# Kernel tuning notes

Measured on AMD Instinct MI355X. Metric: run time of the kernel, lower is better.

The kernel has to match this reference:

```python
import jax, jax.numpy as jnp
import numpy as np

N_HEADS = 16
BLOCK_SIZE = 256


def setup_inputs() -> dict:
    key = jax.random.key(0)
    ks = jax.random.split(key, 5)
    B, T, C = 4, 4096, 1024
    scale = 0.02
    return {
        "x": jax.random.normal(ks[0], (B, T, C), dtype=jnp.float32),
        "Wqkv": jax.random.normal(ks[1], (C, 3 * C), dtype=jnp.float32) * scale,
        "bqkv": jnp.zeros((3 * C,), dtype=jnp.float32),
        "Wout": jax.random.normal(ks[2], (C, C), dtype=jnp.float32) * scale,
        "bout": jnp.zeros((C,), dtype=jnp.float32),
    }


def reference(x, Wqkv, bqkv, Wout, bout):
    B, T, C = x.shape
    H = N_HEADS
    hd = C // H
    bs = BLOCK_SIZE
    nb = T // bs

    qkv = x @ Wqkv + bqkv                     # [B,T,3C]
    qkv = qkv.reshape(B, T, H, 3 * hd).transpose(0, 2, 1, 3)  # [B,H,T,3hd]
    q, k, v = jnp.split(qkv, 3, axis=-1)      # each [B,H,T,hd]

    # block-diagonal local attention: reshape T -> (nb, bs)
    q = q.reshape(B, H, nb, bs, hd)
    k = k.reshape(B, H, nb, bs, hd)
    v = v.reshape(B, H, nb, bs, hd)

    scores = jnp.einsum("bhnqd,bhnkd->bhnqk", q, k) * (hd ** -0.5)
    attn = jax.nn.softmax(scores, axis=-1)
    o = jnp.einsum("bhnqk,bhnkd->bhnqd", attn, v)  # [B,H,nb,bs,hd]

    o = o.reshape(B, H, T, hd).transpose(0, 2, 1, 3).reshape(B, T, C)
    return o @ Wout + bout
```

## Files before the change

### kernel.cpp

```cpp
#include <hip/hip_runtime.h>

typedef unsigned int u32;
typedef unsigned long long u64;
typedef unsigned short u16;
typedef short bf16x8 __attribute__((ext_vector_type(8)));
typedef u16 u16x8 __attribute__((ext_vector_type(8)));
typedef float f32x4 __attribute__((ext_vector_type(4)));


__device__ __forceinline__ u16 f2bf(float f) {
  unsigned u = __float_as_uint(f);
  u += 0x7FFFu + ((u >> 16) & 1u);
  return (u16)(u >> 16);
}

typedef const void __attribute__((address_space(1)))* gas_p;
typedef void __attribute__((address_space(3)))* las_p;

__device__ __forceinline__ void async_ld16(const void* g, void* l) {
  __builtin_amdgcn_global_load_lds((gas_p)g, (las_p)l, 16, 0, 0);
}


__global__ __launch_bounds__(256) void k_prep(const float* __restrict__ x,
                                              u16* __restrict__ xb,
                                              const float* __restrict__ Wqkv,
                                              u16* __restrict__ wqkvT,
                                              const float* __restrict__ Wout,
                                              u16* __restrict__ woT) {
  __shared__ u16 tsh[32][33];
  int bid = blockIdx.x;
  int tid = threadIdx.x;

  if (bid < 8192) {
    int i = bid * 256 + tid;
    const float4* p = (const float4*)x + (size_t)i * 2;
    float4 a = p[0], b = p[1];
    u16x8 o;
    o[0] = f2bf(a.x); o[1] = f2bf(a.y); o[2] = f2bf(a.z); o[3] = f2bf(a.w);
    o[4] = f2bf(b.x); o[5] = f2bf(b.y); o[6] = f2bf(b.z); o[7] = f2bf(b.w);
    *((u16x8*)xb + i) = o;
    return;
  }

  const float* in;
  u16* out;
  int R, Ncols, bx, by;
  if (bid < 11264) {
    int t = bid - 8192;
    in = Wqkv; out = wqkvT; R = 1024; Ncols = 3072;
    bx = t % 96; by = t / 96;
  } else {
    int t = bid - 11264;
    in = Wout; out = woT; R = 1024; Ncols = 1024;
    bx = t & 31; by = t >> 5;
  }
  int tx = tid & 31, ty = tid >> 5;
  int c0 = bx * 32, r0 = by * 32;
#pragma unroll
  for (int j = 0; j < 32; j += 8)
    tsh[ty + j][tx] = f2bf(in[(size_t)(r0 + ty + j) * Ncols + c0 + tx]);
  __syncthreads();
#pragma unroll
  for (int j = 0; j < 32; j += 8)
    out[(size_t)(c0 + ty + j) * R + r0 + tx] = tsh[tx][ty + j];
}


#define STAGE_A2(h_, src_, dd_) do {                                       \
    const u16* g_ = (src_) + (size_t)(h_) * 128 * KK;                      \
    u16* s_ = lds + (dd_) * 16384 + (((h_) * 128 + w * 16) << 6);          \
    async_ld16(g_, s_);                                                    \
    async_ld16(g_ + 8 * (size_t)KK, s_ + 512);                             \
  } while (0)

#define STAGE_B2(h_, src_, dd_) do {                                       \
    const u16* g_ = (src_) + (size_t)(h_) * 128 * KK;                      \
    u16* s_ = lds + 32768 + (dd_) * 16384 + (((h_) * 128 + w * 16) << 6);  \
    async_ld16(g_, s_);                                                    \
    async_ld16(g_ + 8 * (size_t)KK, s_ + 512);                             \
  } while (0)

#define MQUAD(M0, N0)                                                      \
    _Pragma("unroll") for (int ks = 0; ks < 2; ++ks)                       \
    _Pragma("unroll") for (int mm = 0; mm < 4; ++mm)                       \
    _Pragma("unroll") for (int nn = 0; nn < 2; ++nn)                       \
      acc[(M0) + mm][(N0) + nn] = __builtin_amdgcn_mfma_f32_16x16x32_bf16( \
          a[(M0) + mm][ks], b[(N0) + nn][ks], acc[(M0) + mm][(N0) + nn], 0, 0, 0);

#define TBX(d_, bS_, aS_)                                                  \
  {                                                                        \
    const int doA = (d_) * 16384, doB = 32768 + (d_) * 16384;              \
      \
    _Pragma("unroll") for (int f = 0; f < 8; ++f) {                        \
      a[f][0] = *(const bf16x8*)(lds + doA + rAoff + f * 1024 + c0);       \
      a[f][1] = *(const bf16x8*)(lds + doA + rAoff + f * 1024 + c1);       \
    }                                                                      \
    _Pragma("unroll") for (int f = 0; f < 4; ++f) {                        \
      b[f][0] = *(const bf16x8*)(lds + doB + rBoff + f * 1024 + c0);       \
      b[f][1] = *(const bf16x8*)(lds + doB + rBoff + f * 1024 + c1);       \
    }                                                                      \
        \
    STAGE_B2(0, bS_, (d_) ^ 1);                                            \
    STAGE_B2(1, bS_, (d_) ^ 1);                                            \
                            \
    __builtin_amdgcn_s_setprio(1);                                         \
    MQUAD(0, 0)                                                            \
    MQUAD(4, 0)                                                            \
    __builtin_amdgcn_s_setprio(0);                                         \
        \
    __builtin_amdgcn_s_barrier();                                          \
    STAGE_A2(0, aS_, (d_));                                                \
    STAGE_A2(1, aS_, (d_));                                                \
    __builtin_amdgcn_s_setprio(1);                                         \
    MQUAD(0, 2)                                                            \
    MQUAD(4, 2)                                                            \
    __builtin_amdgcn_s_setprio(0);                                         \
    \
    asm volatile("s_waitcnt vmcnt(4)");                                    \
    __builtin_amdgcn_s_barrier();           \
  }

#define EPI(PM0, PN0) do {                                                      \
    int ccol0 = (PN0) + wn * 64 + (lane & 15);                                  \
    float bv0 = bias[ccol0], bv1 = bias[ccol0 + 16];                            \
    float bv2 = bias[ccol0 + 32], bv3 = bias[ccol0 + 48];                       \
    size_t crow0 = (size_t)((PM0) + wm * 128 + ((lane >> 4) << 2));             \
    _Pragma("unroll") for (int m = 0; m < 8; ++m)                               \
    _Pragma("unroll") for (int reg = 0; reg < 4; ++reg) {                       \
      size_t ro = (crow0 + m * 16 + reg) * (size_t)N + ccol0;                   \
      float v0 = acc[m][0][reg] + bv0, v1 = acc[m][1][reg] + bv1;               \
      float v2 = acc[m][2][reg] + bv2, v3 = acc[m][3][reg] + bv3;               \
      if (OUT_BF16) {                                                           \
        ((u16*)Cout)[ro] = f2bf(v0); ((u16*)Cout)[ro + 16] = f2bf(v1);          \
        ((u16*)Cout)[ro + 32] = f2bf(v2); ((u16*)Cout)[ro + 48] = f2bf(v3);     \
      } else {                                                                  \
        ((float*)Cout)[ro] = v0; ((float*)Cout)[ro + 16] = v1;                  \
        ((float*)Cout)[ro + 32] = v2; ((float*)Cout)[ro + 48] = v3;             \
      }                                                                         \
    }                                                                           \
  } while (0)

#define TILE_COORD(tt, mm0, nn0) do {                                           \
    int q_ = nwg >> 3, r_ = nwg & 7, x_ = (tt) & 7, loc_ = (tt) >> 3;           \
    int swz_ = (x_ < r_ ? x_ * (q_ + 1) : r_ * (q_ + 1) + (x_ - r_) * q_) + loc_;\
    mm0 = (swz_ / nbn) << 8; nn0 = (swz_ % nbn) << 8;                           \
  } while (0)

#define ZERO_ACC do {                                                           \
    _Pragma("unroll") for (int m = 0; m < 8; ++m)                               \
    _Pragma("unroll") for (int n = 0; n < 4; ++n)                               \
      acc[m][n] = (f32x4){0.f, 0.f, 0.f, 0.f};                                  \
  } while (0)

template <int OUT_BF16, int KK>
__global__ __launch_bounds__(512, 2) void k_gemm8(const u16* __restrict__ A,
                                                  const u16* __restrict__ Bt,
                                                  const float* __restrict__ bias,
                                                  void* __restrict__ Cout,
                                                  int M, int N) {
  extern __shared__ u16 lds[];
  const int NT = KK / 64;

  int nbn = N >> 8, nbm = M >> 8, nwg = nbm * nbn;
  int tid = threadIdx.x;
  int w = tid >> 6, lane = tid & 63;
  int wm = w >> 2, wn = w & 3;

  int rAoff = (wm * 128 + (lane & 15)) << 6;
  int rBoff = (wn * 64 + (lane & 15)) << 6;
  int hi8 = (lane >> 4) << 3, key8 = (lane & 7) << 3;
  int c0 = hi8 ^ key8;
  int c1 = (32 | hi8) ^ key8;
  int rowoff = w * 16 + (lane >> 3);
  int soff = ((lane & 7) ^ (lane >> 3)) << 3;

  bf16x8 a[8][2], b[4][2];
  f32x4 acc[8][4];

  int t = blockIdx.x;
  int m0, n0;
  TILE_COORD(t, m0, n0);
  const u16* pAg = A + (size_t)(m0 + rowoff) * KK + soff;
  const u16* pBg = Bt + (size_t)(n0 + rowoff) * KK + soff;

  STAGE_A2(0, pAg, 0); STAGE_A2(1, pAg, 0);
  STAGE_B2(0, pBg, 0); STAGE_B2(1, pBg, 0);
  STAGE_A2(0, pAg + 64, 1); STAGE_A2(1, pAg + 64, 1);
  asm volatile("s_waitcnt vmcnt(4)");
  __builtin_amdgcn_s_barrier();
  ZERO_ACC;

  for (;;) {
    int tn = t + gridDim.x;
    bool last = tn >= nwg;
    const u16 *pAgN, *pBgN;
    int m0N = m0, n0N = n0;
    if (last) {
      pAgN = pAg; pBgN = pBg;
    } else {
      TILE_COORD(tn, m0N, n0N);
      pAgN = A + (size_t)(m0N + rowoff) * KK + soff;
      pBgN = Bt + (size_t)(n0N + rowoff) * KK + soff;
    }

    for (int k = 0; k < NT; k += 2) {
      const u16* bS1 = pBg + (k + 1) * 64;
      const u16* aS2 = (k + 2 < NT) ? pAg + (k + 2) * 64 : pAgN + (k + 2 - NT) * 64;
      TBX(0, bS1, aS2)
      const u16* bS2 = (k + 2 < NT) ? pBg + (k + 2) * 64 : pBgN + (k + 2 - NT) * 64;
      const u16* aS3 = (k + 3 < NT) ? pAg + (k + 3) * 64 : pAgN + (k + 3 - NT) * 64;
      TBX(1, bS2, aS3)
    }

    EPI(m0, n0);
    if (last) break;
    t = tn; m0 = m0N; n0 = n0N; pAg = pAgN; pBg = pBgN;
    ZERO_ACC;
  }
  asm volatile("s_waitcnt vmcnt(0) lgkmcnt(0)");
}


__global__ __launch_bounds__(512, 4) void k_attn3(const u16* __restrict__ qkv,
                                                  u16* __restrict__ o) {
  __shared__ u16 ldsK[256 * 64];
  __shared__ u16 ldsV[64 * 256];

  int bid = blockIdx.x;
  int g = ((bid & 7) << 8) | (bid >> 3);
  int hq = g & 1, blk = (g >> 1) & 15, h = (g >> 5) & 15, b = g >> 9;

  int tid = threadIdx.x;
  int w = tid >> 6, lane = tid & 63;
  int hgrp = lane >> 4;
  size_t rowb = ((size_t)(b * 4096 + blk * 256)) * 3072 + (size_t)h * 192;

  int qrow = hq * 128 + w * 16 + (lane & 15);
  const u16* qp = qkv + rowb + (size_t)qrow * 3072 + hgrp * 8;
  bf16x8 qf0 = *(const bf16x8*)(qp);
  bf16x8 qf1 = *(const bf16x8*)(qp + 32);

#pragma unroll
  for (int it = 0; it < 4; ++it) {
    int trow = it * 64 + (tid >> 3);
    const u16* ksrc = qkv + rowb + (size_t)trow * 3072 + 64 +
                      (((lane & 7) ^ (lane >> 3)) << 3);
    async_ld16(ksrc, ldsK + (it * 64 + w * 8) * 64);
  }

  {
    int tg = tid >> 3, d0 = (tid & 7) << 3;
    const u16* vsrc = qkv + rowb + (size_t)(4 * tg) * 3072 + 128 + d0;
    union { uint4 v; u16 s[8]; } r0, r1, r2, r3;
    r0.v = *(const uint4*)(vsrc);
    r1.v = *(const uint4*)(vsrc + 3072);
    r2.v = *(const uint4*)(vsrc + 6144);
    r3.v = *(const uint4*)(vsrc + 9216);
    int gb = ((tg >> 1) << 4) + ((tg & 1) << 3);
#pragma unroll
    for (int c = 0; c < 8; ++c) {
      int d = d0 + c;
      int key = (((d & 7) ^ ((d >> 3) & 7)) & 7) << 4;
      u64 pack = (u64)r0.s[c] | ((u64)r1.s[c] << 16) |
                 ((u64)r2.s[c] << 32) | ((u64)r3.s[c] << 48);
      *(u64*)((char*)ldsV + d * 512 + ((gb & ~15) ^ key) + (gb & 8)) = pack;
    }
  }
  __syncthreads();

  f32x4 acc0[16] = {};
  int cb = hgrp << 4;
#pragma unroll
  for (int ct = 0; ct < 16; ++ct) {
    int krow = ct * 16 + (lane & 15);
    const char* kb = (const char*)ldsK + krow * 128;
    int key = (krow & 7) << 4;
    bf16x8 k0 = *(const bf16x8*)(kb + (cb ^ key));
    bf16x8 k1 = *(const bf16x8*)(kb + ((64 + cb) ^ key));
    acc0[ct] = __builtin_amdgcn_mfma_f32_16x16x32_bf16(k0, qf0, acc0[ct], 0, 0, 0);
    acc0[ct] = __builtin_amdgcn_mfma_f32_16x16x32_bf16(k1, qf1, acc0[ct], 0, 0, 0);
  }

  const float SC = 0.125f * 1.44269504f;
  float rden0;
  {
    float mx = -1e30f;
#pragma unroll
    for (int ct = 0; ct < 16; ++ct)
#pragma unroll
      for (int rg = 0; rg < 4; ++rg) mx = fmaxf(mx, acc0[ct][rg]);
    mx = fmaxf(mx, __shfl_xor(mx, 16));
    mx = fmaxf(mx, __shfl_xor(mx, 32));
    float s = 0.f;
#pragma unroll
    for (int ct = 0; ct < 16; ++ct)
#pragma unroll
      for (int rg = 0; rg < 4; ++rg) {
        float p = exp2f((acc0[ct][rg] - mx) * SC);
        acc0[ct][rg] = p;
        s += p;
      }
    s += __shfl_xor(s, 16);
    s += __shfl_xor(s, 32);
    rden0 = 1.f / s;
  }

  int s1 = (lane & 15) + ((lane >> 4) & 1) * 32;
  int s2 = s1 + 16;
  bool lo = (lane < 32);
  f32x4 oa[4] = {};
#pragma unroll
  for (int kt = 0; kt < 8; ++kt) {
    u32 wA0, wB0, wA1, wB1;
    asm("v_cvt_pk_bf16_f32 %0, %1, %2" : "=v"(wA0)
        : "v"(acc0[2 * kt][0]), "v"(acc0[2 * kt][1]));
    asm("v_cvt_pk_bf16_f32 %0, %1, %2" : "=v"(wB0)
        : "v"(acc0[2 * kt][2]), "v"(acc0[2 * kt][3]));
    asm("v_cvt_pk_bf16_f32 %0, %1, %2" : "=v"(wA1)
        : "v"(acc0[2 * kt + 1][0]), "v"(acc0[2 * kt + 1][1]));
    asm("v_cvt_pk_bf16_f32 %0, %1, %2" : "=v"(wB1)
        : "v"(acc0[2 * kt + 1][2]), "v"(acc0[2 * kt + 1][3]));
    u32 t0a = (u32)__shfl((int)wA0, s1), t0b = (u32)__shfl((int)wA1, s1);
    u32 t1a = (u32)__shfl((int)wB0, s1), t1b = (u32)__shfl((int)wB1, s1);
    u32 t2a = (u32)__shfl((int)wA0, s2), t2b = (u32)__shfl((int)wA1, s2);
    u32 t3a = (u32)__shfl((int)wB0, s2), t3b = (u32)__shfl((int)wB1, s2);
    union { u32 w[4]; bf16x8 v; } pu;
    pu.w[0] = lo ? t0a : t0b;
    pu.w[1] = lo ? t1a : t1b;
    pu.w[2] = lo ? t2a : t2b;
    pu.w[3] = lo ? t3a : t3b;
    bf16x8 pa = pu.v;
    int vkb = 2 * (kt * 32 + hgrp * 8);
#pragma unroll
    for (int nt = 0; nt < 4; ++nt) {
      int vd = nt * 16 + (lane & 15);
      int key = (((vd & 7) ^ ((vd >> 3) & 7)) & 7) << 4;
      bf16x8 vf = *(const bf16x8*)((char*)ldsV + vd * 512 + (vkb ^ key));
      oa[nt] = __builtin_amdgcn_mfma_f32_16x16x32_bf16(pa, vf, oa[nt], 0, 0, 0);
    }
  }

  float rd0[4];
#pragma unroll
  for (int rg = 0; rg < 4; ++rg) rd0[rg] = __shfl(rden0, 4 * hgrp + rg, 16);
  size_t ob = ((size_t)(b * 4096 + blk * 256 + hq * 128 + w * 16)) * 1024 +
              (size_t)h * 64;
#pragma unroll
  for (int nt = 0; nt < 4; ++nt)
#pragma unroll
    for (int rg = 0; rg < 4; ++rg) {
      int col = nt * 16 + (lane & 15);
      o[ob + (size_t)(4 * hgrp + rg) * 1024 + col] = f2bf(oa[nt][rg] * rd0[rg]);
    }
}


extern "C" void kernel_launch(void* const* d_in, const int* in_sizes, int n_in,
                              void* d_out, int out_size, void* d_ws, size_t ws_size,
                              hipStream_t stream) {
  (void)in_sizes; (void)n_in; (void)out_size; (void)ws_size;
  const float* x = (const float*)d_in[0];
  const float* Wqkv = (const float*)d_in[1];
  const float* bqkv = (const float*)d_in[2];
  const float* Wout = (const float*)d_in[3];
  const float* bout = (const float*)d_in[4];
  float* out = (float*)d_out;

  char* ws = (char*)d_ws;
  u16* xb    = (u16*)(ws + 0);
  u16* wqkvT = (u16*)(ws + 33554432);
  u16* woT   = (u16*)(ws + 39845888);
  u16* qkv   = (u16*)(ws + 41943040);
  u16* ob    = (u16*)(ws + 142606336);

  hipFuncSetAttribute(reinterpret_cast<const void*>(&k_gemm8<1, 1024>),
                      hipFuncAttributeMaxDynamicSharedMemorySize, 131072);
  hipFuncSetAttribute(reinterpret_cast<const void*>(&k_gemm8<0, 1024>),
                      hipFuncAttributeMaxDynamicSharedMemorySize, 131072);

  k_prep<<<12288, 256, 0, stream>>>(x, xb, Wqkv, wqkvT, Wout, woT);

  k_gemm8<1, 1024><<<256, 512, 131072, stream>>>(xb, wqkvT, bqkv, qkv, 16384, 3072);

  k_attn3<<<2048, 512, 0, stream>>>(qkv, ob);

  k_gemm8<0, 1024><<<256, 512, 131072, stream>>>(ob, woT, bout, out, 16384, 1024);
}
```

Measured before the change: 234.2 us.

## Rework GEMM to 4 waves with 128x128 per-wave tiles and staged LDS pipeline

Replaces the 8-wave 256x256 GEMM workgroup with a 4-wave version in which each wave computes a 128x128 output sub-tile (8x8 accumulator fragments). The K-step is split into four MFMA quadrants, with A/B fragment reloads and async global-to-LDS stages interleaved between barriers. The goal is more MFMA work per LDS fragment load and less per-wave overhead. The cost is a doubled accumulator register footprint with one workgroup per CU, which lowers occupancy and makes latency hiding depend on the hand-written interleaving.

```diff
diff --git a/kernel.cpp b/kernel.cpp
--- a/kernel.cpp
+++ b/kernel.cpp
@@ -67,76 +67,85 @@
 }
 
 
-#define STAGE_A2(h_, src_, dd_) do {                                       \
-    const u16* g_ = (src_) + (size_t)(h_) * 128 * KK;                      \
-    u16* s_ = lds + (dd_) * 16384 + (((h_) * 128 + w * 16) << 6);          \
-    async_ld16(g_, s_);                                                    \
-    async_ld16(g_ + 8 * (size_t)KK, s_ + 512);                             \
-  } while (0)
-
-#define STAGE_B2(h_, src_, dd_) do {                                       \
-    const u16* g_ = (src_) + (size_t)(h_) * 128 * KK;                      \
-    u16* s_ = lds + 32768 + (dd_) * 16384 + (((h_) * 128 + w * 16) << 6);  \
-    async_ld16(g_, s_);                                                    \
-    async_ld16(g_ + 8 * (size_t)KK, s_ + 512);                             \
-  } while (0)
-
-#define MQUAD(M0, N0)                                                      \
-    _Pragma("unroll") for (int ks = 0; ks < 2; ++ks)                       \
-    _Pragma("unroll") for (int mm = 0; mm < 4; ++mm)                       \
-    _Pragma("unroll") for (int nn = 0; nn < 2; ++nn)                       \
-      acc[(M0) + mm][(N0) + nn] = __builtin_amdgcn_mfma_f32_16x16x32_bf16( \
-          a[(M0) + mm][ks], b[(N0) + nn][ks], acc[(M0) + mm][(N0) + nn], 0, 0, 0);
-
-#define TBX(d_, bS_, aS_)                                                  \
-  {                                                                        \
-    const int doA = (d_) * 16384, doB = 32768 + (d_) * 16384;              \
-      \
-    _Pragma("unroll") for (int f = 0; f < 8; ++f) {                        \
-      a[f][0] = *(const bf16x8*)(lds + doA + rAoff + f * 1024 + c0);       \
-      a[f][1] = *(const bf16x8*)(lds + doA + rAoff + f * 1024 + c1);       \
-    }                                                                      \
-    _Pragma("unroll") for (int f = 0; f < 4; ++f) {                        \
-      b[f][0] = *(const bf16x8*)(lds + doB + rBoff + f * 1024 + c0);       \
-      b[f][1] = *(const bf16x8*)(lds + doB + rBoff + f * 1024 + c1);       \
-    }                                                                      \
+#define STAGE_A4(h_, src_, dd_) do {                                          \
+    _Pragma("unroll") for (int i_ = 0; i_ < 4; ++i_)                          \
+      async_ld16((src_) + (size_t)((h_) * 128 + i_ * 8) * KK,                 \
+                 lds + (dd_) * 16384 + (((h_) * 128 + w * 32 + i_ * 8) << 6));\
+  } while (0)
+
+#define STAGE_B4(h_, src_, dd_) do {                                          \
+    _Pragma("unroll") for (int i_ = 0; i_ < 4; ++i_)                          \
+      async_ld16((src_) + (size_t)((h_) * 128 + i_ * 8) * KK,                 \
+                 lds + 32768 + (dd_) * 16384 +                                \
+                     (((h_) * 128 + w * 32 + i_ * 8) << 6));                  \
+  } while (0)
+
+#define MQ(M0, N0)                                                            \
+    __builtin_amdgcn_s_setprio(1);                                            \
+    _Pragma("unroll") for (int ks = 0; ks < 2; ++ks)                          \
+    _Pragma("unroll") for (int mm = 0; mm < 4; ++mm)                          \
+    _Pragma("unroll") for (int nn = 0; nn < 4; ++nn)                          \
+      acc[(M0) + mm][(N0) + nn] = __builtin_amdgcn_mfma_f32_16x16x32_bf16(    \
+          a[(M0) + mm][ks], b[nn][ks], acc[(M0) + mm][(N0) + nn], 0, 0, 0);   \
+    __builtin_amdgcn_s_setprio(0);
+
+#define TBX(d_, bS_, aS_)                                                     \
+  {                                                                           \
+    const int doA = (d_) * 16384, doB = 32768 + (d_) * 16384;                 \
+                              \
+    _Pragma("unroll") for (int f = 0; f < 4; ++f) {                           \
+      a[f][0] = *(const bf16x8*)(lds + doA + rAoff + f * 1024 + c0);          \
+      a[f][1] = *(const bf16x8*)(lds + doA + rAoff + f * 1024 + c1);          \
+    }                                                                         \
+    _Pragma("unroll") for (int f = 0; f < 4; ++f) {                           \
+      b[f][0] = *(const bf16x8*)(lds + doB + rBoff + f * 1024 + c0);          \
+      b[f][1] = *(const bf16x8*)(lds + doB + rBoff + f * 1024 + c1);          \
+    }                                                                         \
+    STAGE_B4(0, bS_, (d_) ^ 1);                                               \
+    asm volatile("s_waitcnt lgkmcnt(8)");                                     \
+    __builtin_amdgcn_s_barrier();                                             \
+    asm volatile("s_waitcnt lgkmcnt(0)");                                     \
+    MQ(0, 0)                                                                  \
+    __builtin_amdgcn_s_barrier();                                             \
+                                          \
+    _Pragma("unroll") for (int f = 4; f < 8; ++f) {                           \
+      a[f][0] = *(const bf16x8*)(lds + doA + rAoff + f * 1024 + c0);          \
+      a[f][1] = *(const bf16x8*)(lds + doA + rAoff + f * 1024 + c1);          \
+    }                                                                         \
+    STAGE_B4(1, bS_, (d_) ^ 1);                                               \
+    __builtin_amdgcn_s_barrier();                                             \
+    asm volatile("s_waitcnt lgkmcnt(0)");                                     \
+    MQ(4, 0)                                                                  \
+    __builtin_amdgcn_s_barrier();                                             \
+                      \
+    _Pragma("unroll") for (int f = 0; f < 4; ++f) {                           \
+      b[f][0] = *(const bf16x8*)(lds + doB + rBoff + (f + 4) * 1024 + c0);    \
+      b[f][1] = *(const bf16x8*)(lds + doB + rBoff + (f + 4) * 1024 + c1);    \
+    }                                                                         \
+    STAGE_A4(0, aS_, (d_));                                                   \
+    __builtin_amdgcn_s_barrier();                                             \
+    asm volatile("s_waitcnt lgkmcnt(0)");                                     \
+    MQ(4, 4)                                                                  \
+    __builtin_amdgcn_s_barrier();                                             \
         \
-    STAGE_B2(0, bS_, (d_) ^ 1);                                            \
-    STAGE_B2(1, bS_, (d_) ^ 1);                                            \
-                            \
-    __builtin_amdgcn_s_setprio(1);                                         \
-    MQUAD(0, 0)                                                            \
-    MQUAD(4, 0)                                                            \
-    __builtin_amdgcn_s_setprio(0);                                         \
-        \
-    __builtin_amdgcn_s_barrier();                                          \
-    STAGE_A2(0, aS_, (d_));                                                \
-    STAGE_A2(1, aS_, (d_));                                                \
-    __builtin_amdgcn_s_setprio(1);                                         \
-    MQUAD(0, 2)                                                            \
-    MQUAD(4, 2)                                                            \
-    __builtin_amdgcn_s_setprio(0);                                         \
-    \
-    asm volatile("s_waitcnt vmcnt(4)");                                    \
-    __builtin_amdgcn_s_barrier();           \
+    STAGE_A4(1, aS_, (d_));                                                   \
+    MQ(0, 4)                                                                  \
+    asm volatile("s_waitcnt vmcnt(8)");                                       \
+    __builtin_amdgcn_s_barrier();                                             \
   }
 
 #define EPI(PM0, PN0) do {                                                      \
-    int ccol0 = (PN0) + wn * 64 + (lane & 15);                                  \
-    float bv0 = bias[ccol0], bv1 = bias[ccol0 + 16];                            \
-    float bv2 = bias[ccol0 + 32], bv3 = bias[ccol0 + 48];                       \
+    int ccol0 = (PN0) + wn * 128 + (lane & 15);                                 \
+    float bv[8];                                                                \
+    _Pragma("unroll") for (int n = 0; n < 8; ++n) bv[n] = bias[ccol0 + n * 16]; \
     size_t crow0 = (size_t)((PM0) + wm * 128 + ((lane >> 4) << 2));             \
     _Pragma("unroll") for (int m = 0; m < 8; ++m)                               \
     _Pragma("unroll") for (int reg = 0; reg < 4; ++reg) {                       \
       size_t ro = (crow0 + m * 16 + reg) * (size_t)N + ccol0;                   \
-      float v0 = acc[m][0][reg] + bv0, v1 = acc[m][1][reg] + bv1;               \
-      float v2 = acc[m][2][reg] + bv2, v3 = acc[m][3][reg] + bv3;               \
-      if (OUT_BF16) {                                                           \
-        ((u16*)Cout)[ro] = f2bf(v0); ((u16*)Cout)[ro + 16] = f2bf(v1);          \
-        ((u16*)Cout)[ro + 32] = f2bf(v2); ((u16*)Cout)[ro + 48] = f2bf(v3);     \
-      } else {                                                                  \
-        ((float*)Cout)[ro] = v0; ((float*)Cout)[ro + 16] = v1;                  \
-        ((float*)Cout)[ro + 32] = v2; ((float*)Cout)[ro + 48] = v3;             \
+      _Pragma("unroll") for (int n = 0; n < 8; ++n) {                           \
+        float v = acc[m][n][reg] + bv[n];                                       \
+        if (OUT_BF16) ((u16*)Cout)[ro + n * 16] = f2bf(v);                      \
+        else          ((float*)Cout)[ro + n * 16] = v;                          \
       }                                                                         \
     }                                                                           \
   } while (0)
@@ -149,34 +158,34 @@
 
 #define ZERO_ACC do {                                                           \
     _Pragma("unroll") for (int m = 0; m < 8; ++m)                               \
-    _Pragma("unroll") for (int n = 0; n < 4; ++n)                               \
+    _Pragma("unroll") for (int n = 0; n < 8; ++n)                               \
       acc[m][n] = (f32x4){0.f, 0.f, 0.f, 0.f};                                  \
   } while (0)
 
 template <int OUT_BF16, int KK>
-__global__ __launch_bounds__(512, 2) void k_gemm8(const u16* __restrict__ A,
-                                                  const u16* __restrict__ Bt,
-                                                  const float* __restrict__ bias,
-                                                  void* __restrict__ Cout,
-                                                  int M, int N) {
+__global__ __launch_bounds__(256, 1) void k_gemm4w(const u16* __restrict__ A,
+                                                   const u16* __restrict__ Bt,
+                                                   const float* __restrict__ bias,
+                                                   void* __restrict__ Cout,
+                                                   int M, int N) {
   extern __shared__ u16 lds[];
   const int NT = KK / 64;
 
   int nbn = N >> 8, nbm = M >> 8, nwg = nbm * nbn;
   int tid = threadIdx.x;
   int w = tid >> 6, lane = tid & 63;
-  int wm = w >> 2, wn = w & 3;
+  int wm = w >> 1, wn = w & 1;
 
   int rAoff = (wm * 128 + (lane & 15)) << 6;
-  int rBoff = (wn * 64 + (lane & 15)) << 6;
+  int rBoff = (wn * 128 + (lane & 15)) << 6;
   int hi8 = (lane >> 4) << 3, key8 = (lane & 7) << 3;
   int c0 = hi8 ^ key8;
   int c1 = (32 | hi8) ^ key8;
-  int rowoff = w * 16 + (lane >> 3);
+  int rowoff = w * 32 + (lane >> 3);
   int soff = ((lane & 7) ^ (lane >> 3)) << 3;
 
   bf16x8 a[8][2], b[4][2];
-  f32x4 acc[8][4];
+  f32x4 acc[8][8];
 
   int t = blockIdx.x;
   int m0, n0;
@@ -184,10 +193,10 @@
   const u16* pAg = A + (size_t)(m0 + rowoff) * KK + soff;
   const u16* pBg = Bt + (size_t)(n0 + rowoff) * KK + soff;
 
-  STAGE_A2(0, pAg, 0); STAGE_A2(1, pAg, 0);
-  STAGE_B2(0, pBg, 0); STAGE_B2(1, pBg, 0);
-  STAGE_A2(0, pAg + 64, 1); STAGE_A2(1, pAg + 64, 1);
-  asm volatile("s_waitcnt vmcnt(4)");
+  STAGE_A4(0, pAg, 0); STAGE_A4(1, pAg, 0);
+  STAGE_B4(0, pBg, 0); STAGE_B4(1, pBg, 0);
+  STAGE_A4(0, pAg + 64, 1); STAGE_A4(1, pAg + 64, 1);
+  asm volatile("s_waitcnt vmcnt(8)");
   __builtin_amdgcn_s_barrier();
   ZERO_ACC;
 
@@ -374,16 +383,16 @@
   u16* qkv   = (u16*)(ws + 41943040);
   u16* ob    = (u16*)(ws + 142606336);
 
-  hipFuncSetAttribute(reinterpret_cast<const void*>(&k_gemm8<1, 1024>),
+  hipFuncSetAttribute(reinterpret_cast<const void*>(&k_gemm4w<1, 1024>),
                       hipFuncAttributeMaxDynamicSharedMemorySize, 131072);
-  hipFuncSetAttribute(reinterpret_cast<const void*>(&k_gemm8<0, 1024>),
+  hipFuncSetAttribute(reinterpret_cast<const void*>(&k_gemm4w<0, 1024>),
                       hipFuncAttributeMaxDynamicSharedMemorySize, 131072);
 
   k_prep<<<12288, 256, 0, stream>>>(x, xb, Wqkv, wqkvT, Wout, woT);
 
-  k_gemm8<1, 1024><<<256, 512, 131072, stream>>>(xb, wqkvT, bqkv, qkv, 16384, 3072);
+  k_gemm4w<1, 1024><<<256, 256, 131072, stream>>>(xb, wqkvT, bqkv, qkv, 16384, 3072);
 
   k_attn3<<<2048, 512, 0, stream>>>(qkv, ob);
 
-  k_gemm8<0, 1024><<<256, 512, 131072, stream>>>(ob, woT, bout, out, 16384, 1024);
-}
+  k_gemm4w<0, 1024><<<256, 256, 131072, stream>>>(ob, woT, bout, out, 16384, 1024);
+}
```

New measurement: 385.4 us. 1.65x slower.
